# Optimization experiments

Measured on AMD Instinct MI355X. Metric: run time of the kernel, lower is better.

Reference implementation:

```python
import jax, jax.numpy as jnp
import numpy as np
import math

B, L, D_MODEL = 4, 2048, 512
EXPAND, D_STATE, D_CONV = 6, 8, 3
D_INNER = EXPAND * D_MODEL            # 3072
DT_RANK = math.ceil(D_MODEL / 16)     # 32
NH = 8
HF = D_MODEL // NH                    # 64


def setup_inputs() -> dict:
    key = jax.random.key(0)
    ks = jax.random.split(key, 16)
    n = lambda k, sh, s=0.02: jax.random.normal(k, sh, dtype=jnp.float32) * s
    return {
        "x": jax.random.normal(ks[0], (B, L, D_MODEL), dtype=jnp.float32),
        "norm_w": jnp.ones((D_MODEL,), jnp.float32),
        "in_proj_w": n(ks[1], (2 * D_INNER, D_MODEL)),
        "conv_w": n(ks[2], (D_INNER, 1, D_CONV), 0.2),
        "conv_b": jnp.zeros((D_INNER,), jnp.float32),
        "x_proj_w": n(ks[3], (DT_RANK + 2 * D_STATE, D_INNER)),
        "dt_head_w": n(ks[4], (D_INNER, DT_RANK)),
        "dt_head_b": jnp.zeros((D_INNER,), jnp.float32),
        "D": jnp.ones((D_INNER,), jnp.float32),
        "reduce_w": n(ks[5], (D_MODEL, D_INNER)),
        "q_net_w": n(ks[6], (D_MODEL, D_MODEL)),
        "gain_q_w": n(ks[7], (D_MODEL, D_MODEL)),
        "gain_k_w": n(ks[8], (D_MODEL, D_MODEL)),
        "alpha": jnp.ones((1,), jnp.float32),
        "beta": jnp.zeros((1,), jnp.float32),
        "qkv_w": n(ks[9], (3 * D_MODEL + NH, D_MODEL)),
        "qkv_b": jnp.zeros((3 * D_MODEL + NH,), jnp.float32),
        "ttt_lr_bias": jnp.zeros((NH,), jnp.float32),
        "W1": n(ks[10], (NH, HF, HF)),
        "b1": jnp.zeros((NH, HF), jnp.float32),
        "token_idx": 1.0 / jnp.arange(1, L + 1, dtype=jnp.float32),
        "token_idx_bias": jnp.zeros((L,), jnp.float32),
        "ttt_ln_w": jnp.ones((NH, HF), jnp.float32),
        "ttt_ln_b": jnp.zeros((NH, HF), jnp.float32),
        "post_norm_w": jnp.ones((D_MODEL,), jnp.float32),
        "post_norm_b": jnp.zeros((D_MODEL,), jnp.float32),
        "wo_w": n(ks[11], (D_MODEL, D_MODEL)),
        "wo_b": jnp.zeros((D_MODEL,), jnp.float32),
    }


def _rmsnorm(x, w, eps=1e-5):
    return x * jax.lax.rsqrt(jnp.mean(x * x, axis=-1, keepdims=True) + eps) * w


def _layernorm(x, w, b, eps=1e-5):
    mu = x.mean(-1, keepdims=True)
    xh = (x - mu) * jax.lax.rsqrt(x.var(-1, keepdims=True) + eps)
    return xh * w + b


def _longhorn_scan(x, z, dt, k, q, dt_b, D):
    # x,z,dt: [B,L,di]; k,q: [B,L,ds].  Online Longhorn recurrence (matches step()).
    def step(s, t):
        x_t, z_t, dt_t, k_t, q_t = t
        dt_t = jax.nn.sigmoid(dt_t + dt_b)
        dt_t = dt_t / (1.0 + dt_t * jnp.sum(k_t * k_t, -1, keepdims=True))
        dB = dt_t[:, :, None] * k_t[:, None, :]                  # [B,di,ds]
        s = s * (1.0 - dB * k_t[:, None, :]) + x_t[:, :, None] * dB
        y_t = jnp.einsum('bdn,bn->bd', s, q_t) + D * x_t
        return s, y_t * jax.nn.silu(z_t)

    s0 = jnp.zeros((x.shape[0], x.shape[2], k.shape[2]), x.dtype)
    xs = tuple(jnp.moveaxis(a, 1, 0) for a in (x, z, dt, k, q))
    _, ys = jax.lax.scan(step, s0, xs)
    return jnp.moveaxis(ys, 0, 1)                                # [B,L,di]


def _ttt(h, qkv_w, qkv_b, ttt_lr_bias, W1, b1, token_idx, token_idx_bias,
         ln_w, ln_b, pn_w, pn_b, wo_w, wo_b, lr_mult=1.0):
    Bh, N, d = h.shape
    proj = h @ qkv_w.T + qkv_b                                   # [B,N,3d+NH]
    XQK, XV, XGate, lr = (proj[..., :d], proj[..., d:2 * d],
                          proj[..., 2 * d:3 * d], proj[..., 3 * d:])

    def heads(a):  # [B,N,d] -> [B*NH,N,HF]
        return a.reshape(Bh, N, NH, HF).transpose(0, 2, 1, 3).reshape(Bh * NH, N, HF)

    XQ = heads(XQK)            # XQ == XK in the source
    XVh = heads(XV)
    ttt_lr = jax.nn.sigmoid(lr + ttt_lr_bias) * lr_mult          # [B,N,NH]
    ttt_lr = jnp.swapaxes(ttt_lr, 0, 1).reshape(N, Bh * NH, 1)   # [N,B*NH,1]
    tok = jnp.maximum(token_idx + token_idx_bias, 0.0)           # [N]

    W1c = jnp.broadcast_to(W1[None], (Bh, NH, HF, HF)).reshape(Bh * NH, HF, HF)
    b1c = jnp.broadcast_to(b1[None], (Bh, NH, HF)).reshape(Bh * NH, HF)
    lnw = jnp.broadcast_to(ln_w[None], (Bh, NH, HF)).reshape(Bh * NH, HF)
    lnb = jnp.broadcast_to(ln_b[None], (Bh, NH, HF)).reshape(Bh * NH, HF)
    eps = 1e-6
    HFf = jnp.float32(HF)

    def step(carry, t):
        W, bb = carry
        xk, xv, lr_t, tok_t = t
        Z1 = jnp.einsum('bf,bfg->bg', xk, W) + bb
        mu = Z1.mean(-1, keepdims=True)
        std = jnp.sqrt(Z1.var(-1, keepdims=True) + eps)
        xh = (Z1 - mu) / std
        # grad of ||LN(Z1) - (XV - XK)||^2 wrt Z1 (ln_fused_l2_bwd)
        go = (lnw * xh + lnb) - (xv - xk)
        gxh = go * lnw
        grad = (HFf * gxh - gxh.sum(-1, keepdims=True)
                - xh * (gxh * xh).sum(-1, keepdims=True)) / (HFf * std)
        eta = lr_t * tok_t                                       # [B*NH,1]
        W = W - eta[:, :, None] * (xk[:, :, None] * grad[:, None, :])
        bb = bb - eta * grad
        Z1q = jnp.einsum('bf,bfg->bg', xk, W) + bb
        mu2 = Z1q.mean(-1, keepdims=True)
        std2 = jnp.sqrt(Z1q.var(-1, keepdims=True) + eps)
        out_t = xk + lnw * (Z1q - mu2) / std2 + lnb
        return (W, bb), out_t

    xs = (jnp.moveaxis(XQ, 1, 0), jnp.moveaxis(XVh, 1, 0), ttt_lr, tok)
    _, ys = jax.lax.scan(step, (W1c, b1c), xs)                   # [N,B*NH,HF]
    xqw = ys.reshape(N, Bh, NH, HF).transpose(1, 0, 2, 3).reshape(Bh, N, d)
    normed = _layernorm(xqw, pn_w, pn_b)
    gated = jax.nn.gelu(XGate, approximate=True) * normed
    return gated @ wo_w.T + wo_b


def reference(x, norm_w, in_proj_w, conv_w, conv_b, x_proj_w, dt_head_w, dt_head_b,
              D, reduce_w, q_net_w, gain_q_w, gain_k_w, alpha, beta,
              qkv_w, qkv_b, ttt_lr_bias, W1, b1, token_idx, token_idx_bias,
              ttt_ln_w, ttt_ln_b, post_norm_w, post_norm_b, wo_w, wo_b):
    residual = x                                   # residual=None in forward
    xn = _rmsnorm(residual, norm_w)
    # ---- Longhorn block ----
    xz = xn @ in_proj_w.T                          # [B,L,2*di]
    xx, z = jnp.split(xz, 2, axis=-1)
    xc = jnp.swapaxes(xx, 1, 2)                    # [B,di,L]
    xc = jax.lax.conv_general_dilated(
        xc, conv_w, (1,), [(D_CONV - 1, 0)],       # causal depthwise conv
        dimension_numbers=('NCH', 'OIH', 'NCH'), feature_group_count=D_INNER)
    xc = jax.nn.silu(xc + conv_b[None, :, None])
    xb = jnp.swapaxes(xc, 1, 2)                    # [B,L,di]
    x_dbl = xb @ x_proj_w.T
    dt = x_dbl[..., :DT_RANK] @ dt_head_w.T        # [B,L,di] (bias added in scan)
    k = x_dbl[..., DT_RANK:DT_RANK + D_STATE]
    q = x_dbl[..., DT_RANK + D_STATE:]
    y = _longhorn_scan(xb, z, dt, k, q, dt_head_b, D)   # h_hidden, [B,L,di]
    # (out_proj output is discarded by PreCoBlock, so not computed)
    h_red = y @ reduce_w.T                          # [B,L,d]
    # ---- TTT corrective branch ----
    c_hidden = _ttt(h_red, qkv_w, qkv_b, ttt_lr_bias, W1, b1, token_idx,
                    token_idx_bias, ttt_ln_w, ttt_ln_b, post_norm_w, post_norm_b,
                    wo_w, wo_b, lr_mult=1.0)
    z_long = h_red @ q_net_w.T
    z_ttt = c_hidden @ q_net_w.T
    gq = h_red @ gain_q_w.T
    gk = h_red @ gain_k_w.T
    # score = mean_i (gq_i . gk_j)/sqrt(d) == (mean_i gq_i) . gk_j / sqrt(d)
    score = jnp.einsum('bd,bld->bl', gq.mean(axis=1), gk) / jnp.sqrt(jnp.float32(D_MODEL))
    gain = jnp.minimum(jax.nn.sigmoid(alpha * score + beta), 0.55)[..., None]
    out = z_long + gain * (z_ttt - z_long)
    return (out, residual, gain)
```

## Files before the change

### kernel.cpp

```cpp
#include <hip/hip_runtime.h>
#include <hip/hip_bf16.h>
#include <cstdint>
#include <cstddef>

#define L_SEQ 2048
#define BATCH 4
#define DM    512
#define DI    3072
#define NROWS (BATCH * L_SEQ)
#define PROJW 1544
#define CTILE 16
#define BDI   (BATCH * DI)
#define SB    64
#define NSB   (L_SEQ / SB)
#define CHT   16
#define LCH   128
#define NLCH  (L_SEQ / LCH)

using bf16 = __hip_bfloat16;

typedef __attribute__((ext_vector_type(8))) short short8v;
typedef __attribute__((ext_vector_type(4))) float f32x4;


__device__ __forceinline__ float sigmoidf_(float x) { return 1.f / (1.f + __expf(-x)); }
__device__ __forceinline__ float us2f(unsigned int u) {
    union { unsigned int i; float f; } c; c.i = u << 16; return c.f;
}
__device__ __forceinline__ bf16  f2b(float f) { return __float2bfloat16(f); }
__device__ __forceinline__ float b2f(bf16 v)  { return __bfloat162float(v); }
__device__ __forceinline__ void st1(float* p, float v) { *p = v; }
__device__ __forceinline__ void st1(bf16* p, float v)  { *p = f2b(v); }

template <int CTRL>
__device__ __forceinline__ float dppadd_(float x) {
    int s = __builtin_amdgcn_update_dpp(0, __builtin_bit_cast(int, x), CTRL, 0xF, 0xF, true);
    return x + __builtin_bit_cast(float, s);
}
__device__ __forceinline__ float wave_sum_u(float x) {
    x = dppadd_<0x111>(x);
    x = dppadd_<0x112>(x);
    x = dppadd_<0x114>(x);
    x = dppadd_<0x118>(x);
    x = dppadd_<0x142>(x);
    x = dppadd_<0x143>(x);
    return __builtin_bit_cast(float,
        __builtin_amdgcn_readlane(__builtin_bit_cast(int, x), 63));
}

__global__ __launch_bounds__(256) void copy4_k(const float4* __restrict__ in,
                                               float4* __restrict__ out, int n) {
    int i = blockIdx.x * 256 + threadIdx.x;
    if (i < n) out[i] = in[i];
}

__global__ __launch_bounds__(256) void cvt_k(const float* __restrict__ in,
                                             bf16* __restrict__ out, int n4) {
    int i = blockIdx.x * 256 + threadIdx.x;
    if (i >= n4) return;
    float4 v = ((const float4*)in)[i];
    out[4 * i + 0] = f2b(v.x);
    out[4 * i + 1] = f2b(v.y);
    out[4 * i + 2] = f2b(v.z);
    out[4 * i + 3] = f2b(v.w);
}

__global__ __launch_bounds__(256) void rmsnorm_k(const float* __restrict__ x,
                                                 const float* __restrict__ w,
                                                 bf16* __restrict__ xn) {
    int r = blockIdx.x, tid = threadIdx.x;
    const float* row = x + (size_t)r * DM;
    float v0 = row[tid], v1 = row[tid + 256];
    float q = v0 * v0 + v1 * v1;
#pragma unroll
    for (int off = 32; off; off >>= 1) q += __shfl_xor(q, off);
    __shared__ float sm[4];
    if ((tid & 63) == 0) sm[tid >> 6] = q;
    __syncthreads();
    q = sm[0] + sm[1] + sm[2] + sm[3];
    float scale = rsqrtf(q * (1.f / 512.f) + 1e-5f);
    bf16* orow = xn + (size_t)r * DM;
    orow[tid]       = f2b(v0 * scale * w[tid]);
    orow[tid + 256] = f2b(v1 * scale * w[tid + 256]);
}

template <int BIAS, typename TC>
__global__ __launch_bounds__(256) void gemm_mfma(const bf16* __restrict__ A, int lda,
                                                 const bf16* __restrict__ Wb, int ldw,
                                                 const float* __restrict__ bias,
                                                 TC* __restrict__ C, int ldc,
                                                 int N, int K) {
    __shared__ __align__(16) bf16 As[128 * 48];
    __shared__ __align__(16) bf16 Ws[128 * 48];
    const int tid = threadIdx.x;
    const int lane = tid & 63;
    const int widx = tid >> 6;
    const int bm = blockIdx.x * 128;
    const int bn = blockIdx.y * 128;
    const int wr = (widx >> 1) * 64;
    const int wc = (widx & 1) * 64;

    f32x4 acc[4][4];
#pragma unroll
    for (int i = 0; i < 4; ++i)
#pragma unroll
        for (int j = 0; j < 4; ++j) acc[i][j] = (f32x4){0.f, 0.f, 0.f, 0.f};

    const int r0 = tid >> 2;
    const int c0 = tid & 3;
    const int frow = lane & 15;
    const int fk = (lane >> 4) * 8;

    int n0 = bn + r0;       if (n0 > N - 1) n0 = N - 1;
    int n1 = bn + r0 + 64;  if (n1 > N - 1) n1 = N - 1;
    const bf16* pa0 = A + (size_t)(bm + r0) * lda + c0 * 8;
    const bf16* pa1 = A + (size_t)(bm + r0 + 64) * lda + c0 * 8;
    const bf16* pb0 = Wb + (size_t)n0 * ldw + c0 * 8;
    const bf16* pb1 = Wb + (size_t)n1 * ldw + c0 * 8;

    for (int k0 = 0; k0 < K; k0 += 32) {
        short8v a0 = *(const short8v*)(pa0 + k0);
        short8v a1 = *(const short8v*)(pa1 + k0);
        short8v b0 = *(const short8v*)(pb0 + k0);
        short8v b1 = *(const short8v*)(pb1 + k0);
        __syncthreads();
        *(short8v*)&As[r0 * 48 + c0 * 8] = a0;
        *(short8v*)&As[(r0 + 64) * 48 + c0 * 8] = a1;
        *(short8v*)&Ws[r0 * 48 + c0 * 8] = b0;
        *(short8v*)&Ws[(r0 + 64) * 48 + c0 * 8] = b1;
        __syncthreads();
        short8v af[4], bg[4];
#pragma unroll
        for (int mi = 0; mi < 4; ++mi)
            af[mi] = *(const short8v*)&As[(wr + mi * 16 + frow) * 48 + fk];
#pragma unroll
        for (int ni = 0; ni < 4; ++ni)
            bg[ni] = *(const short8v*)&Ws[(wc + ni * 16 + frow) * 48 + fk];
#pragma unroll
        for (int mi = 0; mi < 4; ++mi)
#pragma unroll
            for (int ni = 0; ni < 4; ++ni)
                acc[mi][ni] = __builtin_amdgcn_mfma_f32_16x16x32_bf16(
                    af[mi], bg[ni], acc[mi][ni], 0, 0, 0);
    }

#pragma unroll
    for (int ni = 0; ni < 4; ++ni) {
        int col = bn + wc + ni * 16 + (lane & 15);
        if (col < N) {
            float bz = BIAS ? bias[col] : 0.f;
#pragma unroll
            for (int mi = 0; mi < 4; ++mi) {
                int rbase = bm + wr + mi * 16 + (lane >> 4) * 4;
#pragma unroll
                for (int r = 0; r < 4; ++r) {
                    float v = acc[mi][ni][r] + bz;
                    st1(&C[(size_t)(rbase + r) * ldc + col], v);
                }
            }
        }
    }
}

__global__ __launch_bounds__(256) void conv_boundary_k(const bf16* __restrict__ x,
                                                       bf16* __restrict__ side) {
    int idx = blockIdx.x * 256 + threadIdx.x;
    const int total = (L_SEQ / CTILE - 1) * 2 * BDI;
    if (idx >= total) return;
    int col = idx % BDI;
    int rr = idx / BDI;
    int tile = (rr >> 1) + 1;
    int r = rr & 1;
    int b = col / DI, d = col % DI;
    int l = tile * CTILE - 2 + r;
    side[idx] = x[((size_t)b * L_SEQ + l) * DI + d];
}

__global__ __launch_bounds__(256) void conv_tile_k(bf16* __restrict__ x,
                                                   const bf16* __restrict__ side,
                                                   const float* __restrict__ cw,
                                                   const float* __restrict__ cb) {
    int idx = blockIdx.x * 256 + threadIdx.x;
    const int total = (L_SEQ / CTILE) * BDI;
    if (idx >= total) return;
    int col = idx % BDI;
    int tile = idx / BDI;
    int b = col / DI, d = col % DI;
    float w0 = cw[3 * d], w1 = cw[3 * d + 1], w2 = cw[3 * d + 2], bias = cb[d];
    size_t base = ((size_t)b * L_SEQ + tile * CTILE) * DI + d;
    float xm2, xm1;
    if (tile == 0) { xm2 = 0.f; xm1 = 0.f; }
    else {
        const bf16* sp = side + ((size_t)(tile - 1) * 2) * BDI + col;
        xm2 = b2f(sp[0]);
        xm1 = b2f(sp[BDI]);
    }
    float cur = b2f(x[base]);
#pragma unroll
    for (int i = 0; i < CTILE; ++i) {
        float nxt = (i + 1 < CTILE) ? b2f(x[base + (size_t)(i + 1) * DI]) : 0.f;
        float a = bias + w0 * xm2 + w1 * xm1 + w2 * cur;
        x[base + (size_t)i * DI] = f2b(a * sigmoidf_(a));
        xm2 = xm1; xm1 = cur; cur = nxt;
    }
}

__global__ __launch_bounds__(256) void longhorn_p1(const bf16* __restrict__ xb,
                                                   const float* __restrict__ xdbl,
                                                   const float* __restrict__ dtw,
                                                   const float* __restrict__ dtb_v,
                                                   float* __restrict__ pq) {
    int idx = blockIdx.x * 256 + threadIdx.x;
    int ch = idx / BDI;
    int col = idx % BDI;
    int b = col / DI, d = col % DI;
    float w32[32];
#pragma unroll
    for (int i = 0; i < 32; ++i) w32[i] = dtw[d * 32 + i];
    float dtb = dtb_v[d];
    float P[8] = {1.f, 1.f, 1.f, 1.f, 1.f, 1.f, 1.f, 1.f};
    float Q[8] = {0.f, 0.f, 0.f, 0.f, 0.f, 0.f, 0.f, 0.f};
    size_t rbase = ((size_t)b * L_SEQ + ch * LCH) * DI + d;
    const float* xdb = xdbl + ((size_t)b * L_SEQ + ch * LCH) * 48;

    float xv = b2f(xb[rbase]);
    for (int t = 0; t < LCH; ++t) {
        float x_c = xv;
        if (t + 1 < LCH) xv = b2f(xb[rbase + (size_t)(t + 1) * DI]);
        const float* row = xdb + (size_t)t * 48;
        float dt_c = 0.f;
#pragma unroll
        for (int i = 0; i < 32; i += 4) {
            float4 r4 = *(const float4*)(row + i);
            dt_c = fmaf(r4.x, w32[i + 0], dt_c);
            dt_c = fmaf(r4.y, w32[i + 1], dt_c);
            dt_c = fmaf(r4.z, w32[i + 2], dt_c);
            dt_c = fmaf(r4.w, w32[i + 3], dt_c);
        }
        float kq[8];
#pragma unroll
        for (int i = 0; i < 8; i += 4) *(float4*)&kq[i] = *(const float4*)(row + 32 + i);
        float sig = sigmoidf_(dt_c + dtb);
        float ksq = 0.f;
#pragma unroll
        for (int n = 0; n < 8; ++n) ksq = fmaf(kq[n], kq[n], ksq);
        float dts = sig / (1.f + sig * ksq);
#pragma unroll
        for (int n = 0; n < 8; ++n) {
            float dB = dts * kq[n];
            float a = 1.f - dB * kq[n];
            P[n] *= a;
            Q[n] = fmaf(Q[n], a, x_c * dB);
        }
    }
    float* o = pq + (size_t)idx * 16;
#pragma unroll
    for (int n = 0; n < 8; n += 4) {
        *(float4*)(o + n)     = make_float4(P[n], P[n + 1], P[n + 2], P[n + 3]);
        *(float4*)(o + 8 + n) = make_float4(Q[n], Q[n + 1], Q[n + 2], Q[n + 3]);
    }
}

__global__ __launch_bounds__(256) void longhorn_p2(float* __restrict__ pq) {
    int col = blockIdx.x * 256 + threadIdx.x;
    float s[8] = {0.f, 0.f, 0.f, 0.f, 0.f, 0.f, 0.f, 0.f};
    for (int c = 0; c < NLCH; ++c) {
        float* base = pq + ((size_t)c * BDI + col) * 16;
        float P[8], Q[8];
#pragma unroll
        for (int n = 0; n < 8; n += 4) {
            *(float4*)&P[n] = *(const float4*)(base + n);
            *(float4*)&Q[n] = *(const float4*)(base + 8 + n);
        }
#pragma unroll
        for (int n = 0; n < 8; n += 4)
            *(float4*)(base + n) = make_float4(s[n], s[n + 1], s[n + 2], s[n + 3]);
#pragma unroll
        for (int n = 0; n < 8; ++n) s[n] = fmaf(P[n], s[n], Q[n]);
    }
}

__global__ __launch_bounds__(256) void longhorn_p3(bf16* __restrict__ xb_y,
                                                   const bf16* __restrict__ z,
                                                   const float* __restrict__ xdbl,
                                                   const float* __restrict__ dtw,
                                                   const float* __restrict__ dtb_v,
                                                   const float* __restrict__ Dv,
                                                   const float* __restrict__ pq) {
    int idx = blockIdx.x * 256 + threadIdx.x;
    int ch = idx / BDI;
    int col = idx % BDI;
    int b = col / DI, d = col % DI;
    float w32[32];
#pragma unroll
    for (int i = 0; i < 32; ++i) w32[i] = dtw[d * 32 + i];
    float dtb = dtb_v[d], Dd = Dv[d];
    float s[8];
    {
        const float* base = pq + (size_t)idx * 16;
#pragma unroll
        for (int n = 0; n < 8; n += 4) *(float4*)&s[n] = *(const float4*)(base + n);
    }
    size_t rbase = ((size_t)b * L_SEQ + ch * LCH) * DI + d;
    const float* xdb = xdbl + ((size_t)b * L_SEQ + ch * LCH) * 48;

    float xv = b2f(xb_y[rbase]);
    float zv = b2f(z[rbase]);
    for (int t = 0; t < LCH; ++t) {
        float x_c = xv, z_c = zv;
        if (t + 1 < LCH) {
            size_t nidx = rbase + (size_t)(t + 1) * DI;
            xv = b2f(xb_y[nidx]);
            zv = b2f(z[nidx]);
        }
        const float* row = xdb + (size_t)t * 48;
        float dt_c = 0.f;
#pragma unroll
        for (int i = 0; i < 32; i += 4) {
            float4 r4 = *(const float4*)(row + i);
            dt_c = fmaf(r4.x, w32[i + 0], dt_c);
            dt_c = fmaf(r4.y, w32[i + 1], dt_c);
            dt_c = fmaf(r4.z, w32[i + 2], dt_c);
            dt_c = fmaf(r4.w, w32[i + 3], dt_c);
        }
        float kq[16];
#pragma unroll
        for (int i = 0; i < 16; i += 4) *(float4*)&kq[i] = *(const float4*)(row + 32 + i);
        float sig = sigmoidf_(dt_c + dtb);
        float ksq = 0.f;
#pragma unroll
        for (int n = 0; n < 8; ++n) ksq = fmaf(kq[n], kq[n], ksq);
        float dts = sig / (1.f + sig * ksq);
        float y = 0.f;
#pragma unroll
        for (int n = 0; n < 8; ++n) {
            float dB = dts * kq[n];
            s[n] = s[n] * (1.f - dB * kq[n]) + x_c * dB;
            y = fmaf(s[n], kq[8 + n], y);
        }
        y = fmaf(Dd, x_c, y);
        float out = y * (z_c * sigmoidf_(z_c));
        xb_y[rbase + (size_t)t * DI] = f2b(out);
    }
}

__global__ __launch_bounds__(128) void prep_ttt_k(const bf16* __restrict__ proj,
                                                  const float* __restrict__ lr_bias,
                                                  const float* __restrict__ tok_idx,
                                                  const float* __restrict__ tok_bias,
                                                  const float* __restrict__ ln_w,
                                                  const float* __restrict__ ln_b,
                                                  float* __restrict__ xkf,
                                                  float* __restrict__ etav,
                                                  float* __restrict__ q0s) {
    int bh = blockIdx.x >> 4;
    int t = (blockIdx.x & 15) * 128 + threadIdx.x;
    int b = bh >> 3, h = bh & 7;
    const bf16* prow = proj + ((size_t)b * L_SEQ + t) * PROJW;
    const bf16* pk = prow + h * 64;
    const bf16* pv = prow + 512 + h * 64;
    const float* lwp = ln_w + h * 64;
    const float* lbp = ln_b + h * 64;
    float* xo = xkf + ((size_t)bh * L_SEQ + t) * 64;
    float q0 = 0.f;
#pragma unroll
    for (int i = 0; i < 64; i += 8) {
        short8v sk = *(const short8v*)(pk + i);
        short8v sv = *(const short8v*)(pv + i);
        float v[8];
#pragma unroll
        for (int j = 0; j < 8; ++j) {
            float xk = us2f((unsigned short)sk[j]);
            float xv = us2f((unsigned short)sv[j]);
            v[j] = xk;
            q0 = fmaf((lbp[i + j] - xv + xk), lwp[i + j], q0);
        }
        *(float4*)(xo + i)     = make_float4(v[0], v[1], v[2], v[3]);
        *(float4*)(xo + i + 4) = make_float4(v[4], v[5], v[6], v[7]);
    }
    float eta = sigmoidf_(b2f(prow[1536 + h]) + lr_bias[h]) *
                fmaxf(tok_idx[t] + tok_bias[t], 0.f);
    size_t o = (size_t)bh * L_SEQ + t;
    etav[o] = eta;
    q0s[o]  = q0;
}

__global__ __launch_bounds__(64) void gram16_k(const float* __restrict__ xkf,
                                               float* __restrict__ gram) {
    int bh = blockIdx.x >> 7, c16 = blockIdx.x & 127;
    int lane = threadIdx.x;
    __shared__ __align__(16) float xs[16][68];
    const float* src = xkf + ((size_t)bh * L_SEQ + c16 * 16) * 64;
    {
        int r = lane >> 2, cb = (lane & 3) * 16;
#pragma unroll
        for (int j = 0; j < 4; ++j)
            *(float4*)&xs[r][cb + 4 * j] = *(const float4*)(src + (size_t)r * 64 + cb + 4 * j);
    }
    __syncthreads();
    int t = lane >> 2, s0 = lane & 3;
    float* dst = gram + ((size_t)(bh * 128 + c16) * 16 + t) * 16;
#pragma unroll
    for (int jj = 0; jj < 4; ++jj) {
        int s = s0 * 4 + jj;
        float a0 = 0.f, a1 = 0.f, a2 = 0.f, a3 = 0.f;
#pragma unroll
        for (int j = 0; j < 16; ++j) {
            float4 u = *(const float4*)&xs[t][4 * j];
            float4 v = *(const float4*)&xs[s][4 * j];
            a0 = fmaf(u.x, v.x, a0); a1 = fmaf(u.y, v.y, a1);
            a2 = fmaf(u.z, v.z, a2); a3 = fmaf(u.w, v.w, a3);
        }
        dst[s] = (a0 + a1) + (a2 + a3);
    }
}

__global__ __launch_bounds__(64) __attribute__((amdgpu_waves_per_eu(1, 1)))
void ttt_k(const bf16* __restrict__ proj,
           const float* __restrict__ xkf,
           const float* __restrict__ etav,
           const float* __restrict__ q0s,
           const float* __restrict__ gram16,
           const float* __restrict__ W1,
           const float* __restrict__ b1,
           const float* __restrict__ ln_w,
           const float* __restrict__ ln_b,
           bf16* __restrict__ xqw) {
    const int lane = threadIdx.x;
    const int bh = blockIdx.x;
    const int b = bh >> 3, h = bh & 7;

    __shared__ __align__(16) float xkb[2][SB][64];
    __shared__ __align__(16) bf16  xvb[2][SB][64];
    __shared__ __align__(16) float kb[2][4][CHT][CHT];
    __shared__ __align__(16) float sc[2][2][SB];
    __shared__ __align__(16) float zbb[CHT][64];
    __shared__ __align__(16) float z1qb[CHT][64];
    __shared__ __align__(16) float egb[CHT][64];
    __shared__ float mub[CHT];

    float W[64];
#pragma unroll
    for (int f = 0; f < 64; ++f) W[f] = W1[(size_t)(h * 64 + f) * 64 + lane];
    float bvec = b1[h * 64 + lane];
    float lw = ln_w[h * 64 + lane];
    float lb = ln_b[h * 64 + lane];
    float p = lw * lw;

    const float* kfg = xkf + (size_t)bh * L_SEQ * 64;
    const bf16*  pvg = proj + (size_t)b * L_SEQ * PROJW + 512 + h * 64;
    const float* evg = etav + (size_t)bh * L_SEQ;
    const float* qg  = q0s + (size_t)bh * L_SEQ;
    const float* gmg = gram16 + (size_t)bh * 128 * 256;

    auto stage_async = [&](int c, int bi) {
        const int t0g = c * SB;
#pragma unroll
        for (int i = 0; i < 16; ++i) {
            const float* gp = kfg + (size_t)(t0g + 4 * i) * 64 + lane * 4;
            __builtin_amdgcn_global_load_lds(
                (const __attribute__((address_space(1))) void*)gp,
                (__attribute__((address_space(3))) void*)&xkb[bi][4 * i][0], 16, 0, 0);
        }
#pragma unroll
        for (int i = 0; i < 8; ++i) {
            const bf16* gp = pvg + (size_t)(t0g + 8 * i + (lane >> 3)) * PROJW + (lane & 7) * 8;
            __builtin_amdgcn_global_load_lds(
                (const __attribute__((address_space(1))) void*)gp,
                (__attribute__((address_space(3))) void*)&xvb[bi][8 * i][0], 16, 0, 0);
        }
#pragma unroll
        for (int i = 0; i < 4; ++i) {
            const float* gp = gmg + (size_t)c * 1024 + i * 256 + lane * 4;
            __builtin_amdgcn_global_load_lds(
                (const __attribute__((address_space(1))) void*)gp,
                (__attribute__((address_space(3))) void*)(&kb[bi][0][0][0] + i * 256), 16, 0, 0);
        }
        {
            const float* g0 = evg + t0g + lane;
            __builtin_amdgcn_global_load_lds(
                (const __attribute__((address_space(1))) void*)g0,
                (__attribute__((address_space(3))) void*)&sc[bi][0][0], 4, 0, 0);
            const float* g1 = qg + t0g + lane;
            __builtin_amdgcn_global_load_lds(
                (const __attribute__((address_space(1))) void*)g1,
                (__attribute__((address_space(3))) void*)&sc[bi][1][0], 4, 0, 0);
        }
    };
    auto matvec16 = [&](int nbuf, int nt0) {
#pragma unroll 4
        for (int t = 0; t < CHT; ++t) {
            const float4* row = (const float4*)&xkb[nbuf][nt0 + t][0];
            float a0 = 0.f, a1 = 0.f, a2 = 0.f, a3 = 0.f;
#pragma unroll
            for (int j = 0; j < 16; ++j) {
                float4 kv = row[j];
                a0 = fmaf(kv.x, W[4 * j + 0], a0);
                a1 = fmaf(kv.y, W[4 * j + 1], a1);
                a2 = fmaf(kv.z, W[4 * j + 2], a2);
                a3 = fmaf(kv.w, W[4 * j + 3], a3);
            }
            float zb = (a0 + a1) + (a2 + a3) + bvec;
            zbb[t][lane] = zb;
            float m = wave_sum_u(zb) * 0.015625f;
            if (lane == 0) mub[t] = m;
        }
    };

    stage_async(0, 0);
    asm volatile("s_waitcnt vmcnt(0)" ::: "memory");
    __builtin_amdgcn_sched_barrier(0);
    matvec16(0, 0);

    bf16* xq = xqw + ((size_t)b * L_SEQ) * DM + h * 64 + lane;

    for (int c = 0; c < NSB; ++c) {
        const int cur = c & 1;
        if (c + 1 < NSB) stage_async(c + 1, 1 - cur);
#pragma unroll 1
        for (int sub = 0; sub < 4; ++sub) {
            const int t0 = sub * CHT;
            float eg[CHT];
            float bacc = 0.f;
            float4 krA, krB, krC, krD;
            {
                const float4* krow = (const float4*)&kb[cur][sub][0][0];
                krA = krow[0]; krB = krow[1]; krC = krow[2]; krD = krow[3];
            }
            float zb_n = zbb[0][lane];
            float xk_n = xkb[cur][t0 + 0][lane];
            float xv_n = b2f(xvb[cur][t0 + 0][lane]);
            float et_n = sc[cur][0][t0 + 0];
            float q0_n = sc[cur][1][t0 + 0];
            float mu_n = mub[0];
#pragma unroll
            for (int t = 0; t < CHT; ++t) {
                float kr[CHT];
                *(float4*)&kr[0]  = krA;
                *(float4*)&kr[4]  = krB;
                *(float4*)&kr[8]  = krC;
                *(float4*)&kr[12] = krD;
                float zb_v = zb_n;
                float xk_c = xk_n;
                float xv_c = xv_n;
                float eta  = et_n;
                float q0u  = q0_n;
                float muv  = mu_n;
                if (t + 1 < CHT) {
                    const float4* krow = (const float4*)&kb[cur][sub][t + 1][0];
                    krA = krow[0]; krB = krow[1]; krC = krow[2]; krD = krow[3];
                    zb_n = zbb[t + 1][lane];
                    xk_n = xkb[cur][t0 + t + 1][lane];
                    xv_n = b2f(xvb[cur][t0 + t + 1][lane]);
                    et_n = sc[cur][0][t0 + t + 1];
                    q0_n = sc[cur][1][t0 + t + 1];
                    mu_n = mub[t + 1];
                }

                float gg0 = bacc, gg1 = 0.f, gg2 = 0.f, gg3 = 0.f;
#pragma unroll
                for (int s = 0; s < t; ++s) {
                    if ((s & 3) == 0) gg0 = fmaf(kr[s], eg[s], gg0);
                    else if ((s & 3) == 1) gg1 = fmaf(kr[s], eg[s], gg1);
                    else if ((s & 3) == 2) gg2 = fmaf(kr[s], eg[s], gg2);
                    else gg3 = fmaf(kr[s], eg[s], gg3);
                }
                float z1 = zb_v - ((gg0 + gg1) + (gg2 + gg3));
                float d = z1 - muv;
                float q = (lb - xv_c + xk_c) * lw;
                float S2  = wave_sum_u(d * d);
                float PZ1 = wave_sum_u(p * d);
                float PZ2 = wave_sum_u(p * d * d);
                float Q1  = wave_sum_u(q * d);
                float istd = rsqrtf(S2 * 0.015625f + 1e-6f);
                float A_ = fmaf(istd, PZ1, q0u);
                float Bv = fmaf(istd * istd, PZ2, istd * Q1);
                float xh = d * istd;
                float gxh = fmaf(p, xh, q);
                float grad = (64.f * gxh - A_ - xh * Bv) * (istd * 0.015625f);
                float egt = eta * grad;
                eg[t] = egt;
                egb[t][lane] = egt;
                z1qb[t][lane] = fmaf(-eta * (kr[t] + 1.f), grad, z1);
                bacc += egt;
            }
#pragma unroll 4
            for (int t = 0; t < CHT; ++t) {
                float dq = z1qb[t][lane] - mub[t];
                float SQ = wave_sum_u(dq * dq);
                float istd2 = rsqrtf(SQ * 0.015625f + 1e-6f);
                float xk_c = xkb[cur][t0 + t][lane];
                float outv = fmaf(lw, dq * istd2, xk_c + lb);
                xq[(size_t)(c * SB + t0 + t) * DM] = f2b(outv);
            }
            bool last = (c == NSB - 1) && (sub == 3);
            if (!last) {
#pragma unroll 2
                for (int s = 0; s < CHT; ++s) {
                    float egs = egb[s][lane];
                    const float4* row = (const float4*)&xkb[cur][t0 + s][0];
#pragma unroll
                    for (int j = 0; j < 16; ++j) {
                        float4 kv = row[j];
                        W[4 * j + 0] = fmaf(-egs, kv.x, W[4 * j + 0]);
                        W[4 * j + 1] = fmaf(-egs, kv.y, W[4 * j + 1]);
                        W[4 * j + 2] = fmaf(-egs, kv.z, W[4 * j + 2]);
                        W[4 * j + 3] = fmaf(-egs, kv.w, W[4 * j + 3]);
                    }
                }
                bvec -= bacc;
                int nbuf = cur, nt0 = t0 + CHT;
                if (sub == 3) {
                    nbuf = 1 - cur; nt0 = 0;
                    asm volatile("s_waitcnt vmcnt(0)" ::: "memory");
                    __builtin_amdgcn_sched_barrier(0);
                }
                matvec16(nbuf, nt0);
            }
        }
    }
}

__global__ __launch_bounds__(256) void gated_k(const bf16* __restrict__ xqw,
                                               const bf16* __restrict__ proj,
                                               const float* __restrict__ pnw,
                                               const float* __restrict__ pnb,
                                               bf16* __restrict__ gated) {
    int r = blockIdx.x, tid = threadIdx.x;
    const bf16* row = xqw + (size_t)r * DM;
    float v0 = b2f(row[tid]), v1 = b2f(row[tid + 256]);
    float s = v0 + v1, q = v0 * v0 + v1 * v1;
#pragma unroll
    for (int off = 32; off; off >>= 1) {
        s += __shfl_xor(s, off);
        q += __shfl_xor(q, off);
    }
    __shared__ float sm[8];
    if ((tid & 63) == 0) { sm[tid >> 6] = s; sm[4 + (tid >> 6)] = q; }
    __syncthreads();
    s = sm[0] + sm[1] + sm[2] + sm[3];
    q = sm[4] + sm[5] + sm[6] + sm[7];
    float mu = s * (1.f / 512.f);
    float var = q * (1.f / 512.f) - mu * mu;
    float istd = rsqrtf(var + 1e-5f);
    const bf16* grow = proj + (size_t)r * PROJW + 1024;
    bf16* orow = gated + (size_t)r * DM;
#pragma unroll
    for (int e = 0; e < 2; ++e) {
        int c = tid + e * 256;
        float xv = (e == 0) ? v0 : v1;
        float nv = (xv - mu) * istd * pnw[c] + pnb[c];
        float g = b2f(grow[c]);
        float gg = 0.5f * g * (1.f + tanhf(0.7978845608028654f * (g + 0.044715f * g * g * g)));
        orow[c] = f2b(gg * nv);
    }
}

__global__ __launch_bounds__(256) void mean1_k(const float* __restrict__ gq,
                                               float* __restrict__ partial) {
    int blk = blockIdx.x;
    int b = blk >> 4, c = blk & 15;
    int tid = threadIdx.x;
    const float* p = gq + ((size_t)b * L_SEQ + c * 128) * DM + tid * 2;
    float a0 = 0.f, a1 = 0.f;
    for (int l = 0; l < 128; ++l) {
        float2 v = *(const float2*)(p + (size_t)l * DM);
        a0 += v.x; a1 += v.y;
    }
    partial[(size_t)blk * DM + tid * 2]     = a0;
    partial[(size_t)blk * DM + tid * 2 + 1] = a1;
}
__global__ __launch_bounds__(256) void mean2_k(const float* __restrict__ partial,
                                               float* __restrict__ gqm) {
    int t = blockIdx.x * 256 + threadIdx.x;
    if (t >= 2048) return;
    int b = t >> 9, d = t & 511;
    float acc = 0.f;
#pragma unroll
    for (int c = 0; c < 16; ++c) acc += partial[(size_t)(b * 16 + c) * DM + d];
    gqm[t] = acc * (1.f / 2048.f);
}

__global__ __launch_bounds__(64) void final_k(const float* __restrict__ zl,
                                              const float* __restrict__ zt,
                                              const float* __restrict__ gk,
                                              const float* __restrict__ gqm,
                                              const float* __restrict__ alpha,
                                              const float* __restrict__ beta,
                                              float* __restrict__ out,
                                              float* __restrict__ gain_out) {
    int r = blockIdx.x;
    int lane = threadIdx.x;
    int b = r >> 11;
    const float* gkr = gk + (size_t)r * DM;
    const float* gmb = gqm + b * DM;
    float acc = 0.f;
#pragma unroll
    for (int i = 0; i < 8; ++i) acc = fmaf(gmb[lane + 64 * i], gkr[lane + 64 * i], acc);
#pragma unroll
    for (int off = 32; off; off >>= 1) acc += __shfl_xor(acc, off);
    float score = acc * 0.04419417382415922f;
    float g = sigmoidf_(alpha[0] * score + beta[0]);
    g = fminf(g, 0.55f);
    if (lane == 0) gain_out[r] = g;
    const float* zlr = zl + (size_t)r * DM;
    const float* ztr = zt + (size_t)r * DM;
    float* orow = out + (size_t)r * DM;
#pragma unroll
    for (int i = 0; i < 8; ++i) {
        int c = lane + 64 * i;
        float a = zlr[c];
        orow[c] = a + g * (ztr[c] - a);
    }
}


extern "C" void kernel_launch(void* const* d_in, const int* in_sizes, int n_in,
                              void* d_out, int out_size, void* d_ws, size_t ws_size,
                              hipStream_t stream) {
    const float* x           = (const float*)d_in[0];
    const float* norm_w      = (const float*)d_in[1];
    const float* in_proj_w   = (const float*)d_in[2];
    const float* conv_w      = (const float*)d_in[3];
    const float* conv_b      = (const float*)d_in[4];
    const float* x_proj_w    = (const float*)d_in[5];
    const float* dt_head_w   = (const float*)d_in[6];
    const float* dt_head_b   = (const float*)d_in[7];
    const float* Dvec        = (const float*)d_in[8];
    const float* reduce_w    = (const float*)d_in[9];
    const float* q_net_w     = (const float*)d_in[10];
    const float* gain_q_w    = (const float*)d_in[11];
    const float* gain_k_w    = (const float*)d_in[12];
    const float* alpha       = (const float*)d_in[13];
    const float* beta        = (const float*)d_in[14];
    const float* qkv_w       = (const float*)d_in[15];
    const float* qkv_b       = (const float*)d_in[16];
    const float* ttt_lr_bias = (const float*)d_in[17];
    const float* W1          = (const float*)d_in[18];
    const float* b1          = (const float*)d_in[19];
    const float* token_idx   = (const float*)d_in[20];
    const float* token_bias  = (const float*)d_in[21];
    const float* ttt_ln_w    = (const float*)d_in[22];
    const float* ttt_ln_b    = (const float*)d_in[23];
    const float* post_norm_w = (const float*)d_in[24];
    const float* post_norm_b = (const float*)d_in[25];
    const float* wo_w        = (const float*)d_in[26];
    const float* wo_b        = (const float*)d_in[27];

    const size_t SZ_ROWDM = (size_t)NROWS * DM;
    const size_t MB = 1024u * 1024u;
    char* base = (char*)d_ws;

    float* out_p  = (float*)d_out;
    float* res_p  = out_p + SZ_ROWDM;
    float* gain_p = out_p + 2 * SZ_ROWDM;

    copy4_k<<<(int)(SZ_ROWDM / 4 / 256), 256, 0, stream>>>(
        (const float4*)x, (float4*)res_p, (int)(SZ_ROWDM / 4));

    if (ws_size < 116 * MB) return;

    bf16*  ws0   = (bf16*)base;
    bf16*  xn    = (bf16*)(base + 7 * MB);
    bf16*  h_red = xn;
    bf16*  cside = (bf16*)(base + 7 * MB);
    float* lpq   = (float*)base;
    bf16*  bufX  = (bf16*)(base + 16 * MB);
    bf16*  bufZ  = (bf16*)(base + 64 * MB);
    float* xdbl  = (float*)(base + 112 * MB);
    float* gqm   = (float*)(base + 113 * MB + 512 * 1024);
    float* mpart = (float*)(base + 114 * MB);
    bf16*  proj  = bufX;
    bf16*  xqw   = bufZ;
    bf16*  gated = (bf16*)(base + 72 * MB);
    bf16*  chid  = (bf16*)(base + 80 * MB);
    float* gramb = (float*)(base + 88 * MB);
    float* zlong = (float*)(base + 88 * MB);
    float* xkf   = (float*)(base + 42 * MB);
    float* etav  = (float*)(base + 58 * MB);
    float* q0s   = (float*)(base + 58 * MB + 512 * 1024);
    float* zttt  = (float*)(base + 42 * MB);
    float* gq    = (float*)(base + 16 * MB);
    float* gk    = (float*)(base + 64 * MB);

    rmsnorm_k<<<NROWS, 256, 0, stream>>>(x, norm_w, xn);

    cvt_k<<<(2 * DI * DM / 4 + 255) / 256, 256, 0, stream>>>(in_proj_w, ws0, 2 * DI * DM / 4);
    {
        dim3 g(NROWS / 128, DI / 128);
        gemm_mfma<0, bf16><<<g, 256, 0, stream>>>(xn, DM, ws0, DM, nullptr, bufX, DI, DI, DM);
        gemm_mfma<0, bf16><<<g, 256, 0, stream>>>(xn, DM, ws0 + (size_t)DI * DM, DM, nullptr, bufZ, DI, DI, DM);
    }

    conv_boundary_k<<<((L_SEQ / CTILE - 1) * 2 * BDI) / 256, 256, 0, stream>>>(bufX, cside);
    conv_tile_k<<<((L_SEQ / CTILE) * BDI) / 256, 256, 0, stream>>>(bufX, cside, conv_w, conv_b);

    cvt_k<<<(48 * DI / 4 + 255) / 256, 256, 0, stream>>>(x_proj_w, ws0, 48 * DI / 4);
    {
        dim3 g(NROWS / 128, 1);
        gemm_mfma<0, float><<<g, 256, 0, stream>>>(bufX, DI, ws0, DI, nullptr, xdbl, 48, 48, DI);
    }

    longhorn_p1<<<(NLCH * BDI) / 256, 256, 0, stream>>>(bufX, xdbl, dt_head_w, dt_head_b, lpq);
    longhorn_p2<<<BDI / 256, 256, 0, stream>>>(lpq);
    longhorn_p3<<<(NLCH * BDI) / 256, 256, 0, stream>>>(bufX, bufZ, xdbl, dt_head_w,
                                                        dt_head_b, Dvec, lpq);

    cvt_k<<<(DM * DI / 4 + 255) / 256, 256, 0, stream>>>(reduce_w, ws0, DM * DI / 4);
    {
        dim3 g(NROWS / 128, DM / 128);
        gemm_mfma<0, bf16><<<g, 256, 0, stream>>>(bufX, DI, ws0, DI, nullptr, h_red, DM, DM, DI);
    }

    cvt_k<<<(PROJW * DM / 4 + 255) / 256, 256, 0, stream>>>(qkv_w, ws0, PROJW * DM / 4);
    {
        dim3 g(NROWS / 128, (PROJW + 127) / 128);
        gemm_mfma<1, bf16><<<g, 256, 0, stream>>>(h_red, DM, ws0, DM, qkv_b, proj, PROJW, PROJW, DM);
    }

    prep_ttt_k<<<32 * 16, 128, 0, stream>>>(proj, ttt_lr_bias, token_idx, token_bias,
                                            ttt_ln_w, ttt_ln_b, xkf, etav, q0s);
    gram16_k<<<32 * 128, 64, 0, stream>>>(xkf, gramb);
    ttt_k<<<BATCH * 8, 64, 0, stream>>>(proj, xkf, etav, q0s, gramb, W1, b1,
                                        ttt_ln_w, ttt_ln_b, xqw);

    gated_k<<<NROWS, 256, 0, stream>>>(xqw, proj, post_norm_w, post_norm_b, gated);

    cvt_k<<<(DM * DM / 4 + 255) / 256, 256, 0, stream>>>(wo_w, ws0, DM * DM / 4);
    {
        dim3 g(NROWS / 128, DM / 128);
        gemm_mfma<1, bf16><<<g, 256, 0, stream>>>(gated, DM, ws0, DM, wo_b, chid, DM, DM, DM);
    }

    cvt_k<<<(DM * DM / 4 + 255) / 256, 256, 0, stream>>>(q_net_w, ws0, DM * DM / 4);
    {
        dim3 g(NROWS / 128, DM / 128);
        gemm_mfma<0, float><<<g, 256, 0, stream>>>(h_red, DM, ws0, DM, nullptr, zlong, DM, DM, DM);
        gemm_mfma<0, float><<<g, 256, 0, stream>>>(chid, DM, ws0, DM, nullptr, zttt, DM, DM, DM);
    }

    cvt_k<<<(DM * DM / 4 + 255) / 256, 256, 0, stream>>>(gain_q_w, ws0, DM * DM / 4);
    {
        dim3 g(NROWS / 128, DM / 128);
        gemm_mfma<0, float><<<g, 256, 0, stream>>>(h_red, DM, ws0, DM, nullptr, gq, DM, DM, DM);
    }
    cvt_k<<<(DM * DM / 4 + 255) / 256, 256, 0, stream>>>(gain_k_w, ws0, DM * DM / 4);
    {
        dim3 g(NROWS / 128, DM / 128);
        gemm_mfma<0, float><<<g, 256, 0, stream>>>(h_red, DM, ws0, DM, nullptr, gk, DM, DM, DM);
    }

    mean1_k<<<64, 256, 0, stream>>>(gq, mpart);
    mean2_k<<<8, 256, 0, stream>>>(mpart, gqm);
    final_k<<<NROWS, 64, 0, stream>>>(zlong, zttt, gk, gqm, alpha, beta, out_p, gain_p);
}
```

Before: 2.355 ms.

## Overlap TTT scan with concatenated h_red GEMMs in one heterogeneous kernel

Folds the TTT recurrence and a single concatenated GEMM of h_red against q_net, gain_q and gain_k into one launch. The first 32 blocks run the sequential TTT body on one wave while the remaining blocks compute the three projections, so the mostly idle GPU during the latency-bound scan does useful GEMM work. It also fuses the residual copy into rmsnorm, converts three weight matrices with one kernel, and stores the z_long, z_ttt, gq and gk intermediates as bf16 instead of fp32, which cuts memory traffic but lowers precision. The TTT blocks now launch with 256 threads, which may change occupancy and register allocation for that latency-critical path.

```diff
diff --git a/kernel.cpp b/kernel.cpp
--- a/kernel.cpp
+++ b/kernel.cpp
@@ -65,9 +65,23 @@
     out[4 * i + 3] = f2b(v.w);
 }
 
-__global__ __launch_bounds__(256) void rmsnorm_k(const float* __restrict__ x,
-                                                 const float* __restrict__ w,
-                                                 bf16* __restrict__ xn) {
+__global__ __launch_bounds__(256) void cvt3_k(const float* __restrict__ a,
+                                              const float* __restrict__ b,
+                                              const float* __restrict__ c,
+                                              bf16* __restrict__ out) {
+    int i = blockIdx.x * 256 + threadIdx.x;
+    const int seg = 512 * 512 / 4;
+    const float* src = (i < seg) ? a : (i < 2 * seg) ? b : c;
+    int j = (i < seg) ? i : (i < 2 * seg) ? i - seg : i - 2 * seg;
+    float4 v = ((const float4*)src)[j];
+    bf16* o = out + (size_t)i * 4;
+    o[0] = f2b(v.x); o[1] = f2b(v.y); o[2] = f2b(v.z); o[3] = f2b(v.w);
+}
+
+__global__ __launch_bounds__(256) void rmsnorm_res_k(const float* __restrict__ x,
+                                                     const float* __restrict__ w,
+                                                     bf16* __restrict__ xn,
+                                                     float* __restrict__ res) {
     int r = blockIdx.x, tid = threadIdx.x;
     const float* row = x + (size_t)r * DM;
     float v0 = row[tid], v1 = row[tid + 256];
@@ -80,8 +94,11 @@
     q = sm[0] + sm[1] + sm[2] + sm[3];
     float scale = rsqrtf(q * (1.f / 512.f) + 1e-5f);
     bf16* orow = xn + (size_t)r * DM;
+    float* rrow = res + (size_t)r * DM;
     orow[tid]       = f2b(v0 * scale * w[tid]);
     orow[tid + 256] = f2b(v1 * scale * w[tid + 256]);
+    rrow[tid]       = v0;
+    rrow[tid + 256] = v1;
 }
 
 template <int BIAS, typename TC>
@@ -415,17 +432,16 @@
     }
 }
 
-__global__ __launch_bounds__(64) __attribute__((amdgpu_waves_per_eu(1, 1)))
-void ttt_k(const bf16* __restrict__ proj,
-           const float* __restrict__ xkf,
-           const float* __restrict__ etav,
-           const float* __restrict__ q0s,
-           const float* __restrict__ gram16,
-           const float* __restrict__ W1,
-           const float* __restrict__ b1,
-           const float* __restrict__ ln_w,
-           const float* __restrict__ ln_b,
-           bf16* __restrict__ xqw) {
+__device__ __forceinline__ void ttt_body(const bf16* __restrict__ proj,
+                                         const float* __restrict__ xkf,
+                                         const float* __restrict__ etav,
+                                         const float* __restrict__ q0s,
+                                         const float* __restrict__ gram16,
+                                         const float* __restrict__ W1,
+                                         const float* __restrict__ b1,
+                                         const float* __restrict__ ln_w,
+                                         const float* __restrict__ ln_b,
+                                         bf16* __restrict__ xqw) {
     const int lane = threadIdx.x;
     const int bh = blockIdx.x;
     const int b = bh >> 3, h = bh & 7;
@@ -621,6 +637,95 @@
     }
 }
 
+__global__ __launch_bounds__(256) void hetero_k(const bf16* __restrict__ proj,
+                                                const float* __restrict__ xkf,
+                                                const float* __restrict__ etav,
+                                                const float* __restrict__ q0s,
+                                                const float* __restrict__ gram16,
+                                                const float* __restrict__ W1,
+                                                const float* __restrict__ b1,
+                                                const float* __restrict__ ln_w,
+                                                const float* __restrict__ ln_b,
+                                                bf16* __restrict__ xqw,
+                                                const bf16* __restrict__ hred,
+                                                const bf16* __restrict__ wcat,
+                                                bf16* __restrict__ zl,
+                                                bf16* __restrict__ gq,
+                                                bf16* __restrict__ gk) {
+    if (blockIdx.x < 32) {
+        if (threadIdx.x < 64)
+            ttt_body(proj, xkf, etav, q0s, gram16, W1, b1, ln_w, ln_b, xqw);
+        return;
+    }
+    __shared__ __align__(16) bf16 As[128 * 48];
+    __shared__ __align__(16) bf16 Ws[128 * 48];
+    const int bidx = blockIdx.x - 32;
+    const int tid = threadIdx.x;
+    const int lane = tid & 63;
+    const int widx = tid >> 6;
+    const int bm = (bidx & 63) * 128;
+    const int bn = (bidx >> 6) * 128;
+    const int wr = (widx >> 1) * 64;
+    const int wc = (widx & 1) * 64;
+
+    f32x4 acc[4][4];
+#pragma unroll
+    for (int i = 0; i < 4; ++i)
+#pragma unroll
+        for (int j = 0; j < 4; ++j) acc[i][j] = (f32x4){0.f, 0.f, 0.f, 0.f};
+
+    const int r0 = tid >> 2;
+    const int c0 = tid & 3;
+    const int frow = lane & 15;
+    const int fk = (lane >> 4) * 8;
+
+    const bf16* pa0 = hred + (size_t)(bm + r0) * DM + c0 * 8;
+    const bf16* pa1 = hred + (size_t)(bm + r0 + 64) * DM + c0 * 8;
+    const bf16* pb0 = wcat + (size_t)(bn + r0) * DM + c0 * 8;
+    const bf16* pb1 = wcat + (size_t)(bn + r0 + 64) * DM + c0 * 8;
+
+    for (int k0 = 0; k0 < DM; k0 += 32) {
+        short8v a0 = *(const short8v*)(pa0 + k0);
+        short8v a1 = *(const short8v*)(pa1 + k0);
+        short8v b0 = *(const short8v*)(pb0 + k0);
+        short8v b1 = *(const short8v*)(pb1 + k0);
+        __syncthreads();
+        *(short8v*)&As[r0 * 48 + c0 * 8] = a0;
+        *(short8v*)&As[(r0 + 64) * 48 + c0 * 8] = a1;
+        *(short8v*)&Ws[r0 * 48 + c0 * 8] = b0;
+        *(short8v*)&Ws[(r0 + 64) * 48 + c0 * 8] = b1;
+        __syncthreads();
+        short8v af[4], bg[4];
+#pragma unroll
+        for (int mi = 0; mi < 4; ++mi)
+            af[mi] = *(const short8v*)&As[(wr + mi * 16 + frow) * 48 + fk];
+#pragma unroll
+        for (int ni = 0; ni < 4; ++ni)
+            bg[ni] = *(const short8v*)&Ws[(wc + ni * 16 + frow) * 48 + fk];
+#pragma unroll
+        for (int mi = 0; mi < 4; ++mi)
+#pragma unroll
+            for (int ni = 0; ni < 4; ++ni)
+                acc[mi][ni] = __builtin_amdgcn_mfma_f32_16x16x32_bf16(
+                    af[mi], bg[ni], acc[mi][ni], 0, 0, 0);
+    }
+
+#pragma unroll
+    for (int ni = 0; ni < 4; ++ni) {
+        int col = bn + wc + ni * 16 + (lane & 15);
+        int buf = col >> 9;
+        int lc = col & 511;
+        bf16* Cb = (buf == 0) ? zl : (buf == 1) ? gq : gk;
+#pragma unroll
+        for (int mi = 0; mi < 4; ++mi) {
+            int rbase = bm + wr + mi * 16 + (lane >> 4) * 4;
+#pragma unroll
+            for (int r = 0; r < 4; ++r)
+                Cb[(size_t)(rbase + r) * 512 + lc] = f2b(acc[mi][ni][r]);
+        }
+    }
+}
+
 __global__ __launch_bounds__(256) void gated_k(const bf16* __restrict__ xqw,
                                                const bf16* __restrict__ proj,
                                                const float* __restrict__ pnw,
@@ -656,16 +761,16 @@
     }
 }
 
-__global__ __launch_bounds__(256) void mean1_k(const float* __restrict__ gq,
+__global__ __launch_bounds__(256) void mean1_k(const bf16* __restrict__ gq,
                                                float* __restrict__ partial) {
     int blk = blockIdx.x;
     int b = blk >> 4, c = blk & 15;
     int tid = threadIdx.x;
-    const float* p = gq + ((size_t)b * L_SEQ + c * 128) * DM + tid * 2;
+    const bf16* p = gq + ((size_t)b * L_SEQ + c * 128) * DM + tid * 2;
     float a0 = 0.f, a1 = 0.f;
     for (int l = 0; l < 128; ++l) {
-        float2 v = *(const float2*)(p + (size_t)l * DM);
-        a0 += v.x; a1 += v.y;
+        ushort2 u = *(const ushort2*)(p + (size_t)l * DM);
+        a0 += us2f(u.x); a1 += us2f(u.y);
     }
     partial[(size_t)blk * DM + tid * 2]     = a0;
     partial[(size_t)blk * DM + tid * 2 + 1] = a1;
@@ -681,9 +786,9 @@
     gqm[t] = acc * (1.f / 2048.f);
 }
 
-__global__ __launch_bounds__(64) void final_k(const float* __restrict__ zl,
-                                              const float* __restrict__ zt,
-                                              const float* __restrict__ gk,
+__global__ __launch_bounds__(64) void final_k(const bf16* __restrict__ zl,
+                                              const bf16* __restrict__ zt,
+                                              const bf16* __restrict__ gk,
                                               const float* __restrict__ gqm,
                                               const float* __restrict__ alpha,
                                               const float* __restrict__ beta,
@@ -692,25 +797,25 @@
     int r = blockIdx.x;
     int lane = threadIdx.x;
     int b = r >> 11;
-    const float* gkr = gk + (size_t)r * DM;
+    const bf16* gkr = gk + (size_t)r * DM;
     const float* gmb = gqm + b * DM;
     float acc = 0.f;
 #pragma unroll
-    for (int i = 0; i < 8; ++i) acc = fmaf(gmb[lane + 64 * i], gkr[lane + 64 * i], acc);
+    for (int i = 0; i < 8; ++i) acc = fmaf(gmb[lane + 64 * i], b2f(gkr[lane + 64 * i]), acc);
 #pragma unroll
     for (int off = 32; off; off >>= 1) acc += __shfl_xor(acc, off);
     float score = acc * 0.04419417382415922f;
     float g = sigmoidf_(alpha[0] * score + beta[0]);
     g = fminf(g, 0.55f);
     if (lane == 0) gain_out[r] = g;
-    const float* zlr = zl + (size_t)r * DM;
-    const float* ztr = zt + (size_t)r * DM;
+    const bf16* zlr = zl + (size_t)r * DM;
+    const bf16* ztr = zt + (size_t)r * DM;
     float* orow = out + (size_t)r * DM;
 #pragma unroll
     for (int i = 0; i < 8; ++i) {
         int c = lane + 64 * i;
-        float a = zlr[c];
-        orow[c] = a + g * (ztr[c] - a);
+        float a = b2f(zlr[c]);
+        orow[c] = a + g * (b2f(ztr[c]) - a);
     }
 }
 
@@ -755,12 +860,15 @@
     float* res_p  = out_p + SZ_ROWDM;
     float* gain_p = out_p + 2 * SZ_ROWDM;
 
-    copy4_k<<<(int)(SZ_ROWDM / 4 / 256), 256, 0, stream>>>(
-        (const float4*)x, (float4*)res_p, (int)(SZ_ROWDM / 4));
-
-    if (ws_size < 116 * MB) return;
+    if (ws_size < 116 * MB) {
+        copy4_k<<<(int)(SZ_ROWDM / 4 / 256), 256, 0, stream>>>(
+            (const float4*)x, (float4*)res_p, (int)(SZ_ROWDM / 4));
+        return;
+    }
 
     bf16*  ws0   = (bf16*)base;
+    bf16*  wcat  = (bf16*)base;
+    bf16*  wob16 = (bf16*)(base + 2 * MB);
     bf16*  xn    = (bf16*)(base + 7 * MB);
     bf16*  h_red = xn;
     bf16*  cside = (bf16*)(base + 7 * MB);
@@ -772,18 +880,18 @@
     float* mpart = (float*)(base + 114 * MB);
     bf16*  proj  = bufX;
     bf16*  xqw   = bufZ;
-    bf16*  gated = (bf16*)(base + 72 * MB);
-    bf16*  chid  = (bf16*)(base + 80 * MB);
+    bf16*  zl    = (bf16*)(base + 72 * MB);
+    bf16*  gq    = (bf16*)(base + 80 * MB);
     float* gramb = (float*)(base + 88 * MB);
-    float* zlong = (float*)(base + 88 * MB);
+    bf16*  gk    = (bf16*)(base + 92 * MB);
+    bf16*  zttt  = (bf16*)(base + 100 * MB);
+    bf16*  gated = (bf16*)(base + 104 * MB);
+    bf16*  chid  = (bf16*)(base + 42 * MB);
     float* xkf   = (float*)(base + 42 * MB);
     float* etav  = (float*)(base + 58 * MB);
     float* q0s   = (float*)(base + 58 * MB + 512 * 1024);
-    float* zttt  = (float*)(base + 42 * MB);
-    float* gq    = (float*)(base + 16 * MB);
-    float* gk    = (float*)(base + 64 * MB);
-
-    rmsnorm_k<<<NROWS, 256, 0, stream>>>(x, norm_w, xn);
+
+    rmsnorm_res_k<<<NROWS, 256, 0, stream>>>(x, norm_w, xn, res_p);
 
     cvt_k<<<(2 * DI * DM / 4 + 255) / 256, 256, 0, stream>>>(in_proj_w, ws0, 2 * DI * DM / 4);
     {
@@ -821,36 +929,22 @@
     prep_ttt_k<<<32 * 16, 128, 0, stream>>>(proj, ttt_lr_bias, token_idx, token_bias,
                                             ttt_ln_w, ttt_ln_b, xkf, etav, q0s);
     gram16_k<<<32 * 128, 64, 0, stream>>>(xkf, gramb);
-    ttt_k<<<BATCH * 8, 64, 0, stream>>>(proj, xkf, etav, q0s, gramb, W1, b1,
-                                        ttt_ln_w, ttt_ln_b, xqw);
+    cvt3_k<<<3 * 256, 256, 0, stream>>>(q_net_w, gain_q_w, gain_k_w, wcat);
+
+    hetero_k<<<32 + 768, 256, 0, stream>>>(proj, xkf, etav, q0s, gramb, W1, b1,
+                                           ttt_ln_w, ttt_ln_b, xqw,
+                                           h_red, wcat, zl, gq, gk);
 
     gated_k<<<NROWS, 256, 0, stream>>>(xqw, proj, post_norm_w, post_norm_b, gated);
 
-    cvt_k<<<(DM * DM / 4 + 255) / 256, 256, 0, stream>>>(wo_w, ws0, DM * DM / 4);
+    cvt_k<<<(DM * DM / 4 + 255) / 256, 256, 0, stream>>>(wo_w, wob16, DM * DM / 4);
     {
         dim3 g(NROWS / 128, DM / 128);
-        gemm_mfma<1, bf16><<<g, 256, 0, stream>>>(gated, DM, ws0, DM, wo_b, chid, DM, DM, DM);
-    }
-
-    cvt_k<<<(DM * DM / 4 + 255) / 256, 256, 0, stream>>>(q_net_w, ws0, DM * DM / 4);
-    {
-        dim3 g(NROWS / 128, DM / 128);
-        gemm_mfma<0, float><<<g, 256, 0, stream>>>(h_red, DM, ws0, DM, nullptr, zlong, DM, DM, DM);
-        gemm_mfma<0, float><<<g, 256, 0, stream>>>(chid, DM, ws0, DM, nullptr, zttt, DM, DM, DM);
-    }
-
-    cvt_k<<<(DM * DM / 4 + 255) / 256, 256, 0, stream>>>(gain_q_w, ws0, DM * DM / 4);
-    {
-        dim3 g(NROWS / 128, DM / 128);
-        gemm_mfma<0, float><<<g, 256, 0, stream>>>(h_red, DM, ws0, DM, nullptr, gq, DM, DM, DM);
-    }
-    cvt_k<<<(DM * DM / 4 + 255) / 256, 256, 0, stream>>>(gain_k_w, ws0, DM * DM / 4);
-    {
-        dim3 g(NROWS / 128, DM / 128);
-        gemm_mfma<0, float><<<g, 256, 0, stream>>>(h_red, DM, ws0, DM, nullptr, gk, DM, DM, DM);
+        gemm_mfma<1, bf16><<<g, 256, 0, stream>>>(gated, DM, wob16, DM, wo_b, chid, DM, DM, DM);
+        gemm_mfma<0, bf16><<<g, 256, 0, stream>>>(chid, DM, wcat, DM, nullptr, zttt, DM, DM, DM);
     }
 
     mean1_k<<<64, 256, 0, stream>>>(gq, mpart);
     mean2_k<<<8, 256, 0, stream>>>(mpart, gqm);
-    final_k<<<NROWS, 64, 0, stream>>>(zlong, zttt, gk, gqm, alpha, beta, out_p, gain_p);
-}
+    final_k<<<NROWS, 64, 0, stream>>>(zl, zttt, gk, gqm, alpha, beta, out_p, gain_p);
+}
```

Result: faster. 2.304 ms (-2.2%).
